# Performance work log

Measured on AMD Instinct MI355X. Metric: run time of the kernel, lower is better.

Reference implementation:

```python
import jax, jax.numpy as jnp
import numpy as np

B, T, D = 16, 4096, 768          # batch, tokens, hidden
N_BOX = 1024                      # total boxes across batch
MAX_BBOX = 128                    # cfg.MODEL.MAX_BBOX_NUM
DIM_DETR = 256                    # DETR feature dim (features[:,1:])


def _lin(k, din, dout):
    kw, kb = jax.random.split(k)
    s = 1.0 / np.sqrt(din)
    W = jax.random.uniform(kw, (dout, din), minval=-s, maxval=s, dtype=jnp.float32)
    b = jax.random.uniform(kb, (dout,), minval=-s, maxval=s, dtype=jnp.float32)
    return W, b


def setup_inputs() -> dict:
    key = jax.random.key(0)
    ks = jax.random.split(key, 10)
    inputs = jax.random.normal(ks[0], (B, T, D), dtype=jnp.float32)
    img = jnp.sort(jax.random.randint(ks[1], (N_BOX,), 0, B))
    rest = jax.random.randint(ks[2], (N_BOX, 4), 0, 224)
    bboxes = jnp.concatenate([img[:, None], rest], axis=1).astype(jnp.int32)
    features = jax.random.normal(ks[3], (N_BOX, 1 + DIM_DETR), dtype=jnp.float32)
    t1w, t1b = _lin(ks[4], D, D)      # transform layer 1
    t2w, t2b = _lin(ks[5], D, D)      # transform layer 2
    d1w, d1b = _lin(ks[6], D, D)      # deep_trans layer 1
    d2w, d2b = _lin(ks[7], D, D)      # deep_trans layer 2
    k8a, k8b = jax.random.split(ks[8])
    m1w, m1b = _lin(k8a, DIM_DETR, D) # mlp layer 1 (256->768)
    m2w, m2b = _lin(k8b, D, D)        # mlp layer 2
    pw, pb = _lin(ks[9], 2 * D, D)    # projection (1536->768)
    return dict(inputs=inputs, bboxes=bboxes, features=features,
                t1w=t1w, t1b=t1b, t2w=t2w, t2b=t2b,
                d1w=d1w, d1b=d1b, d2w=d2w, d2b=d2b,
                m1w=m1w, m1b=m1b, m2w=m2w, m2b=m2b,
                pw=pw, pb=pb)


def reference(inputs, bboxes, features, t1w, t1b, t2w, t2b,
              d1w, d1b, d2w, d2b, m1w, m1b, m2w, m2b, pw, pb):
    x = inputs.mean(axis=1)                                    # [B, D]
    ret_x = jax.nn.relu(x @ d1w.T + d1b) @ d2w.T + d2b         # deep_trans
    xt = jax.nn.relu(x @ t1w.T + t1b) @ t2w.T + t2b            # transform
    img = bboxes[:, 0]                                          # [N] image idx per box
    x_boxes = xt[img]                                           # broadcast image feat to its boxes
    fm = jax.nn.relu(features[:, 1:] @ m1w.T + m1b) @ m2w.T + m2b  # DETR mlp
    h = jnp.concatenate([x_boxes, fm], axis=1) @ pw.T + pb      # [N, D]
    # ragged pad: scatter each box into slot (img, rank-within-image)
    counts = jax.ops.segment_sum(jnp.ones((N_BOX,), jnp.int32), img, num_segments=B)
    offsets = jnp.cumsum(counts) - counts                       # exclusive cumsum (boxes sorted by img)
    pos = jnp.arange(N_BOX) - offsets[img]
    vis_output = jnp.zeros((B, MAX_BBOX, D), h.dtype).at[img, pos].set(h)
    att_mask = (jnp.arange(MAX_BBOX)[None, :] < counts[:, None]).astype(jnp.float32)
    return vis_output, att_mask, ret_x
```

## Files before the change

### kernel.cpp

```cpp
#include <hip/hip_runtime.h>

#define B_ 16
#define T_ 4096
#define D_ 768
#define NBOX 1024
#define MAXBB 128
#define DDETR 256

typedef unsigned short u16;
typedef short bf16x8 __attribute__((ext_vector_type(8)));
typedef float f32x4 __attribute__((ext_vector_type(4)));

__device__ __forceinline__ void split_bf(float f, u16& h, u16& l) {
    unsigned u = __builtin_bit_cast(unsigned, f);
    unsigned r = u + 0x7fffu + ((u >> 16) & 1u);
    u16 hb = (u16)(r >> 16);
    float hf = __builtin_bit_cast(float, (unsigned)hb << 16);
    float lf = f - hf;
    unsigned ul = __builtin_bit_cast(unsigned, lf);
    unsigned rl = ul + 0x7fffu + ((ul >> 16) & 1u);
    h = hb; l = (u16)(rl >> 16);
}

__global__ __launch_bounds__(192) void k_mean_partial(const float4* __restrict__ in4,
                                                      float4* __restrict__ part4) {
    int blk = blockIdx.x;
    int b = blk >> 6, c = blk & 63;
    int t = threadIdx.x;
    const float4* base = in4 + (size_t)b * (T_ * D_ / 4) + (size_t)c * (64 * D_ / 4);
    float4 s = {0.f, 0.f, 0.f, 0.f};
    #pragma unroll 4
    for (int r = 0; r < 64; ++r) {
        float4 v = base[(size_t)r * 192 + t];
        s.x += v.x; s.y += v.y; s.z += v.z; s.w += v.w;
    }
    part4[(size_t)blk * 192 + t] = s;
}

struct WDesc { const float* src; u16* hi; u16* lo; int N; int K; int stride; int vec; };
struct WPack8 { WDesc d[8]; };

__global__ __launch_bounds__(256) void k_pack_all(WPack8 ws, const float* __restrict__ part,
                                                  u16* __restrict__ xph, u16* __restrict__ xpl) {
    __shared__ float xm[768];
    if (blockIdx.y == 8) {
        if (blockIdx.x >= 16) return;
        int b = blockIdx.x;
        int t = threadIdx.x;
        if (t < 192) {
            f32x4 s = {0.f, 0.f, 0.f, 0.f};
            #pragma unroll 4
            for (int c = 0; c < 64; ++c)
                s += *(const f32x4*)(part + ((size_t)(b * 64 + c)) * 768 + t * 4);
            s *= (1.0f / T_);
            *(f32x4*)(xm + t * 4) = s;
        }
        __syncthreads();
        if (t < 96) {
            const float* p = xm + t * 8;
            bf16x8 hv, lv;
            #pragma unroll
            for (int j = 0; j < 8; ++j) {
                u16 h, l;
                split_bf(p[j], h, l); hv[j] = (short)h; lv[j] = (short)l;
            }
            size_t off = ((size_t)t * 16 + b) * 8;
            *(bf16x8*)(xph + off) = hv;
            *(bf16x8*)(xpl + off) = lv;
        }
        return;
    }
    WDesc d = ws.d[blockIdx.y];
    int idx = blockIdx.x * 256 + threadIdx.x;
    int Kc = d.K >> 3;
    int total = d.N * Kc;
    if (idx >= total) return;
    int n = idx / Kc, kc = idx - n * Kc;
    const float* s = d.src + (size_t)n * d.stride + kc * 8;
    float v[8];
    if (d.vec) {
        f32x4 v0 = *(const f32x4*)s, v1 = *(const f32x4*)(s + 4);
        #pragma unroll
        for (int j = 0; j < 4; ++j) { v[j] = v0[j]; v[4 + j] = v1[j]; }
    } else {
        #pragma unroll
        for (int j = 0; j < 8; ++j) v[j] = s[j];
    }
    bf16x8 hv, lv;
    #pragma unroll
    for (int j = 0; j < 8; ++j) {
        u16 h, l;
        split_bf(v[j], h, l); hv[j] = (short)h; lv[j] = (short)l;
    }
    size_t off = ((size_t)(n >> 4) * Kc + kc) * 128 + (n & 15) * 8;
    *(bf16x8*)(d.hi + off) = hv;
    *(bf16x8*)(d.lo + off) = lv;
}

template<int GATHER>
__global__ __launch_bounds__(256) void k_mfma(const u16* __restrict__ Ahi, const u16* __restrict__ Alo,
                                              const u16* __restrict__ Whi, const u16* __restrict__ Wlo,
                                              const u16* __restrict__ Xth, const u16* __restrict__ Xtl,
                                              const int* __restrict__ bbx,
                                              float* __restrict__ P, int Kc, int kcLen, int nks) {
    int z = blockIdx.z;
    int term = z / nks, ks = z - term * nks;
    int lane = threadIdx.x & 63, w = threadIdx.x >> 6;
    int wm = w >> 1, wn = w & 1;
    int mt0 = blockIdx.y * 8 + wm * 4;
    int nt0 = blockIdx.x * 8 + wn * 4;
    int kc0 = ks * kcLen;
    int nk = kcLen >> 2;

    const u16* W = (term == 1) ? Wlo : Whi;
    const u16* Wp = W + ((size_t)nt0 * Kc + kc0) * 128 + lane * 8;
    size_t wstr = (size_t)Kc * 128;

    const u16* Abase;
    size_t aofs[4];
    if (GATHER && ks == 0) {
        Abase = (term == 2) ? Xtl : Xth;
        #pragma unroll
        for (int i = 0; i < 4; ++i) {
            int row = (mt0 + i) * 16 + (lane & 15);
            aofs[i] = (size_t)(lane >> 4) * 128 + (size_t)bbx[row * 5] * 8;
        }
    } else {
        int AKc = GATHER ? 96 : Kc;
        int kc0a = GATHER ? 0 : kc0;
        Abase = (term == 2) ? Alo : Ahi;
        #pragma unroll
        for (int i = 0; i < 4; ++i)
            aofs[i] = ((size_t)(mt0 + i) * AKc + kc0a) * 128 + lane * 8;
    }

    bf16x8 a[4], b[4];
    #pragma unroll
    for (int i = 0; i < 4; ++i) {
        a[i] = *(const bf16x8*)(Abase + aofs[i]);
        b[i] = *(const bf16x8*)(Wp + i * wstr);
    }
    f32x4 acc[16];
    #pragma unroll
    for (int i = 0; i < 16; ++i) acc[i] = (f32x4){0.f, 0.f, 0.f, 0.f};

    for (int k = 0; k < nk; ++k) {
        bf16x8 an[4], bn[4];
        if (k + 1 < nk) {
            #pragma unroll
            for (int i = 0; i < 4; ++i) {
                an[i] = *(const bf16x8*)(Abase + aofs[i] + (size_t)(k + 1) * 512);
                bn[i] = *(const bf16x8*)(Wp + i * wstr + (size_t)(k + 1) * 512);
            }
        }
        #pragma unroll
        for (int i = 0; i < 4; ++i)
            #pragma unroll
            for (int j = 0; j < 4; ++j)
                acc[i * 4 + j] = __builtin_amdgcn_mfma_f32_16x16x32_bf16(a[i], b[j], acc[i * 4 + j], 0, 0, 0);
        #pragma unroll
        for (int i = 0; i < 4; ++i) { a[i] = an[i]; b[i] = bn[i]; }
    }

    float* Pz = P + (size_t)z * (1024 * 768);
    int rb = (lane >> 4) * 4, cb = lane & 15;
    #pragma unroll
    for (int i = 0; i < 4; ++i)
        #pragma unroll
        for (int j = 0; j < 4; ++j) {
            int row = (mt0 + i) * 16 + rb;
            int col = (nt0 + j) * 16 + cb;
            float* p = Pz + (size_t)row * 768 + col;
            f32x4 v = acc[i * 4 + j];
            #pragma unroll
            for (int r = 0; r < 4; ++r) p[(size_t)r * 768] = v[r];
        }
}

template<int RELU>
__global__ __launch_bounds__(256) void k_epi_pack(const float* __restrict__ P, int NS,
                                                  const float* __restrict__ bias,
                                                  u16* __restrict__ dhi, u16* __restrict__ dlo,
                                                  int KcDst, int kcOff) {
    int idx = blockIdx.x * 256 + threadIdx.x;
    int m = idx / 96, kc = idx - m * 96;
    const float* p0 = P + (size_t)m * 768 + kc * 8;
    f32x4 s0 = *(const f32x4*)p0, s1 = *(const f32x4*)(p0 + 4);
    for (int z = 1; z < NS; ++z) {
        const float* p = p0 + (size_t)z * (1024 * 768);
        s0 += *(const f32x4*)p; s1 += *(const f32x4*)(p + 4);
    }
    s0 += *(const f32x4*)(bias + kc * 8);
    s1 += *(const f32x4*)(bias + kc * 8 + 4);
    bf16x8 hv, lv;
    #pragma unroll
    for (int j = 0; j < 4; ++j) {
        float v0 = RELU ? fmaxf(s0[j], 0.f) : s0[j];
        float v1 = RELU ? fmaxf(s1[j], 0.f) : s1[j];
        u16 h, l;
        split_bf(v0, h, l); hv[j] = (short)h; lv[j] = (short)l;
        split_bf(v1, h, l); hv[4 + j] = (short)h; lv[4 + j] = (short)l;
    }
    size_t off = ((size_t)(m >> 4) * KcDst + kcOff + kc) * 128 + (m & 15) * 8;
    *(bf16x8*)(dhi + off) = hv;
    *(bf16x8*)(dlo + off) = lv;
}

__global__ __launch_bounds__(256) void k_epi_vis(const float* __restrict__ P, int NS,
                                                 const float* __restrict__ bias,
                                                 float* __restrict__ vis,
                                                 const int* __restrict__ bbx,
                                                 const int* __restrict__ off) {
    int idx = blockIdx.x * 256 + threadIdx.x;
    int m = idx / 192, c4 = idx - m * 192;
    size_t o = (size_t)m * 768 + c4 * 4;
    f32x4 s = *(const f32x4*)(P + o);
    for (int z = 1; z < NS; ++z) s += *(const f32x4*)(P + (size_t)z * (1024 * 768) + o);
    s += *(const f32x4*)(bias + c4 * 4);
    int b = bbx[m * 5];
    int pp = m - off[b];
    if (pp < MAXBB)
        *(f32x4*)&vis[((size_t)(b * MAXBB + pp)) * 768 + c4 * 4] = s;
}

__global__ __launch_bounds__(256) void k_small(const u16* __restrict__ A0h, const u16* __restrict__ A0l,
                                               const u16* __restrict__ A1h, const u16* __restrict__ A1l,
                                               const u16* __restrict__ W0h, const u16* __restrict__ W0l,
                                               const u16* __restrict__ W1h, const u16* __restrict__ W1l,
                                               float* __restrict__ Ps) {
    int z = blockIdx.y;
    int term = z >> 2, ks = z & 3;
    int lane = threadIdx.x & 63, w = threadIdx.x >> 6;
    int nt0 = blockIdx.x * 16 + w * 4;
    int path = nt0 >= 48;
    int ntp = nt0 - path * 48;
    const u16* Ah = path ? A1h : A0h;
    const u16* Al = path ? A1l : A0l;
    const u16* Wh = path ? W1h : W0h;
    const u16* Wl = path ? W1l : W0l;
    const u16* A = (term == 2) ? Al : Ah;
    const u16* W = (term == 1) ? Wl : Wh;
    int kc0 = ks * 24;

    const u16* Ap = A + (size_t)kc0 * 128 + lane * 8;
    const u16* Wp = W + ((size_t)ntp * 96 + kc0) * 128 + lane * 8;

    f32x4 acc[4];
    #pragma unroll
    for (int i = 0; i < 4; ++i) acc[i] = (f32x4){0.f, 0.f, 0.f, 0.f};

    #pragma unroll
    for (int k = 0; k < 6; ++k) {
        bf16x8 a = *(const bf16x8*)(Ap + (size_t)k * 512);
        bf16x8 b[4];
        #pragma unroll
        for (int j = 0; j < 4; ++j)
            b[j] = *(const bf16x8*)(Wp + (size_t)j * 96 * 128 + (size_t)k * 512);
        #pragma unroll
        for (int j = 0; j < 4; ++j)
            acc[j] = __builtin_amdgcn_mfma_f32_16x16x32_bf16(a, b[j], acc[j], 0, 0, 0);
    }

    float* Pz = Ps + (size_t)z * (16 * 1536);
    int rb = (lane >> 4) * 4, cb = lane & 15;
    #pragma unroll
    for (int j = 0; j < 4; ++j) {
        int col = (nt0 + j) * 16 + cb;
        float* p = Pz + (size_t)rb * 1536 + col;
        f32x4 v = acc[j];
        #pragma unroll
        for (int r = 0; r < 4; ++r) p[(size_t)r * 1536] = v[r];
    }
}

__global__ __launch_bounds__(256) void k_sepi1(const float* __restrict__ Ps,
                                               const float* __restrict__ d1b, const float* __restrict__ t1b,
                                               u16* __restrict__ xh, u16* __restrict__ xl) {
    int idx = blockIdx.x * 256 + threadIdx.x;
    int r = idx / 192, cc = idx - r * 192;
    size_t base = (size_t)r * 1536 + cc * 8;
    f32x4 s0 = {0,0,0,0}, s1 = {0,0,0,0};
    for (int z = 0; z < 12; ++z) {
        const float* p = Ps + (size_t)z * (16 * 1536) + base;
        s0 += *(const f32x4*)p; s1 += *(const f32x4*)(p + 4);
    }
    int path = cc >= 96;
    int ccp = cc - path * 96;
    const float* bias = (path ? t1b : d1b) + ccp * 8;
    s0 += *(const f32x4*)bias;
    s1 += *(const f32x4*)(bias + 4);
    bf16x8 hv, lv;
    #pragma unroll
    for (int j = 0; j < 4; ++j) {
        u16 h, l;
        split_bf(fmaxf(s0[j], 0.f), h, l); hv[j] = (short)h; lv[j] = (short)l;
        split_bf(fmaxf(s1[j], 0.f), h, l); hv[4 + j] = (short)h; lv[4 + j] = (short)l;
    }
    size_t off = (size_t)path * 12288 + (size_t)ccp * 128 + r * 8;
    *(bf16x8*)(xh + off) = hv;
    *(bf16x8*)(xl + off) = lv;
}

__global__ __launch_bounds__(256) void k_sepi2(const float* __restrict__ Ps,
                                               const float* __restrict__ d2b, const float* __restrict__ t2b,
                                               float* __restrict__ retx,
                                               u16* __restrict__ xth, u16* __restrict__ xtl) {
    int idx = blockIdx.x * 256 + threadIdx.x;
    int r = idx / 192, cc = idx - r * 192;
    size_t base = (size_t)r * 1536 + cc * 8;
    f32x4 s0 = {0,0,0,0}, s1 = {0,0,0,0};
    for (int z = 0; z < 12; ++z) {
        const float* p = Ps + (size_t)z * (16 * 1536) + base;
        s0 += *(const f32x4*)p; s1 += *(const f32x4*)(p + 4);
    }
    int path = cc >= 96;
    int ccp = cc - path * 96;
    const float* bias = (path ? t2b : d2b) + ccp * 8;
    s0 += *(const f32x4*)bias;
    s1 += *(const f32x4*)(bias + 4);
    if (!path) {
        float* o = retx + (size_t)r * 768 + ccp * 8;
        *(f32x4*)o = s0;
        *(f32x4*)(o + 4) = s1;
    } else {
        bf16x8 hv, lv;
        #pragma unroll
        for (int j = 0; j < 4; ++j) {
            u16 h, l;
            split_bf(s0[j], h, l); hv[j] = (short)h; lv[j] = (short)l;
            split_bf(s1[j], h, l); hv[4 + j] = (short)h; lv[4 + j] = (short)l;
        }
        size_t off = (size_t)ccp * 128 + r * 8;
        *(bf16x8*)(xth + off) = hv;
        *(bf16x8*)(xtl + off) = lv;
    }
}

__global__ __launch_bounds__(256) void k_meta_vz(const int* __restrict__ bboxes,
                                                 int* __restrict__ cnt_g, int* __restrict__ off_g,
                                                 float* __restrict__ att, f32x4* __restrict__ vis4) {
    if (blockIdx.x > 0) {
        int idx = (blockIdx.x - 1) * 256 + threadIdx.x;
        vis4[idx] = (f32x4){0.f, 0.f, 0.f, 0.f};
        return;
    }
    __shared__ int cnt[B_];
    __shared__ int off[B_];
    int tid = threadIdx.x;
    if (tid < B_) cnt[tid] = 0;
    __syncthreads();
    for (int i = tid; i < NBOX; i += 256) atomicAdd(&cnt[bboxes[i * 5]], 1);
    __syncthreads();
    if (tid == 0) {
        int acc = 0;
        for (int b = 0; b < B_; ++b) { off[b] = acc; acc += cnt[b]; }
    }
    __syncthreads();
    if (tid < B_) { cnt_g[tid] = cnt[tid]; off_g[tid] = off[tid]; }
    for (int j = tid; j < B_ * MAXBB; j += 256) {
        int b = j >> 7, p = j & 127;
        att[j] = (p < cnt[b]) ? 1.0f : 0.0f;
    }
}

extern "C" void kernel_launch(void* const* d_in, const int* in_sizes, int n_in,
                              void* d_out, int out_size, void* d_ws, size_t ws_size,
                              hipStream_t stream) {
    const float* inputs   = (const float*)d_in[0];
    const int*   bboxes   = (const int*)d_in[1];
    const float* features = (const float*)d_in[2];
    const float* t1w = (const float*)d_in[3];
    const float* t1b = (const float*)d_in[4];
    const float* t2w = (const float*)d_in[5];
    const float* t2b = (const float*)d_in[6];
    const float* d1w = (const float*)d_in[7];
    const float* d1b = (const float*)d_in[8];
    const float* d2w = (const float*)d_in[9];
    const float* d2b = (const float*)d_in[10];
    const float* m1w = (const float*)d_in[11];
    const float* m1b = (const float*)d_in[12];
    const float* m2w = (const float*)d_in[13];
    const float* m2b = (const float*)d_in[14];
    const float* pw  = (const float*)d_in[15];
    const float* pb  = (const float*)d_in[16];

    float* out  = (float*)d_out;
    float* vis  = out;
    float* att  = out + 1572864;
    float* retx = out + 1574912;

    float* wsf  = (float*)d_ws;
    float* part = wsf;
    float* P    = wsf + 786432;
    float* Ps   = P + 6 * 786432;
    int*   cnt  = (int*)(Ps + 294912);
    int*   off  = cnt + 16;
    u16*   sb   = (u16*)(off + 48);

    u16* t1wh = sb;              u16* t1wl = t1wh + 589824;
    u16* t2wh = t1wl + 589824;   u16* t2wl = t2wh + 589824;
    u16* d1wh = t2wl + 589824;   u16* d1wl = d1wh + 589824;
    u16* d2wh = d1wl + 589824;   u16* d2wl = d2wh + 589824;
    u16* m1wh = d2wl + 589824;   u16* m1wl = m1wh + 196608;
    u16* m2wh = m1wl + 196608;   u16* m2wl = m2wh + 589824;
    u16* pwh  = m2wl + 589824;   u16* pwl  = pwh + 1179648;
    u16* feah = pwl + 1179648;   u16* feal = feah + 262144;
    u16* fm1h = feal + 262144;   u16* fm1l = fm1h + 786432;
    u16* fmh  = fm1l + 786432;   u16* fml  = fmh + 786432;
    u16* xph  = fml + 786432;    u16* xpl  = xph + 12288;
    u16* xch  = xpl + 12288;     u16* xcl  = xch + 24576;
    u16* xth  = xcl + 24576;     u16* xtl  = xth + 12288;

    k_meta_vz<<<1537, 256, 0, stream>>>(bboxes, cnt, off, att, (f32x4*)vis);

    k_mean_partial<<<B_ * 64, 192, 0, stream>>>((const float4*)inputs, (float4*)part);

    WPack8 wp;
    wp.d[0] = {t1w, t1wh, t1wl, 768, 768, 768, 1};
    wp.d[1] = {t2w, t2wh, t2wl, 768, 768, 768, 1};
    wp.d[2] = {d1w, d1wh, d1wl, 768, 768, 768, 1};
    wp.d[3] = {d2w, d2wh, d2wl, 768, 768, 768, 1};
    wp.d[4] = {m1w, m1wh, m1wl, 768, 256, 256, 1};
    wp.d[5] = {m2w, m2wh, m2wl, 768, 768, 768, 1};
    wp.d[6] = {pw,  pwh,  pwl,  768, 1536, 1536, 1};
    wp.d[7] = {features + 1, feah, feal, 1024, 256, 257, 0};
    k_pack_all<<<dim3(576, 9), 256, 0, stream>>>(wp, part, xph, xpl);

    k_small<<<dim3(6, 12), 256, 0, stream>>>(xph, xpl, xph, xpl,
                                             d1wh, d1wl, t1wh, t1wl, Ps);
    k_sepi1<<<12, 256, 0, stream>>>(Ps, d1b, t1b, xch, xcl);
    k_small<<<dim3(6, 12), 256, 0, stream>>>(xch, xcl, xch + 12288, xcl + 12288,
                                             d2wh, d2wl, t2wh, t2wl, Ps);
    k_sepi2<<<12, 256, 0, stream>>>(Ps, d2b, t2b, retx, xth, xtl);

    k_mfma<0><<<dim3(6, 8, 3), 256, 0, stream>>>(feah, feal, m1wh, m1wl,
                                                 nullptr, nullptr, nullptr, P, 32, 32, 1);
    k_epi_pack<1><<<384, 256, 0, stream>>>(P, 3, m1b, fm1h, fm1l, 96, 0);

    k_mfma<0><<<dim3(6, 8, 6), 256, 0, stream>>>(fm1h, fm1l, m2wh, m2wl,
                                                 nullptr, nullptr, nullptr, P, 96, 48, 2);
    k_epi_pack<0><<<384, 256, 0, stream>>>(P, 6, m2b, fmh, fml, 96, 0);

    k_mfma<1><<<dim3(6, 8, 6), 256, 0, stream>>>(fmh, fml, pwh, pwl,
                                                 xth, xtl, bboxes, P, 192, 96, 2);
    k_epi_vis<<<768, 256, 0, stream>>>(P, 6, pb, vis, bboxes, off);
}
```

Measured before the change: 408.8 us.

## Merge independent kernels into phase kernels and drop split-K for MLP GEMMs

Combines the mean-partial, meta/zero-fill and weight-pack kernels into one front kernel, and pairs the small deep/transform GEMMs with the DETR MLP GEMMs and their epilogues in shared phase launches. This cuts the launch count from about 13 to 8 and lets independent work share the GPU. The MFMA GEMMs no longer use split-K, so each block walks the full K range and the partial buffer shrinks to three terms. The gather GEMM now switches between xt and fm sources inside its K loop. The trade-off is fewer blocks per GEMM and longer serial K loops, which may lower parallelism on the big GEMMs.

```diff
diff --git a/kernel.cpp b/kernel.cpp
--- a/kernel.cpp
+++ b/kernel.cpp
@@ -22,56 +22,58 @@
     h = hb; l = (u16)(rl >> 16);
 }
 
-__global__ __launch_bounds__(192) void k_mean_partial(const float4* __restrict__ in4,
-                                                      float4* __restrict__ part4) {
-    int blk = blockIdx.x;
-    int b = blk >> 6, c = blk & 63;
-    int t = threadIdx.x;
-    const float4* base = in4 + (size_t)b * (T_ * D_ / 4) + (size_t)c * (64 * D_ / 4);
-    float4 s = {0.f, 0.f, 0.f, 0.f};
-    #pragma unroll 4
-    for (int r = 0; r < 64; ++r) {
-        float4 v = base[(size_t)r * 192 + t];
-        s.x += v.x; s.y += v.y; s.z += v.z; s.w += v.w;
-    }
-    part4[(size_t)blk * 192 + t] = s;
-}
-
 struct WDesc { const float* src; u16* hi; u16* lo; int N; int K; int stride; int vec; };
 struct WPack8 { WDesc d[8]; };
 
-__global__ __launch_bounds__(256) void k_pack_all(WPack8 ws, const float* __restrict__ part,
-                                                  u16* __restrict__ xph, u16* __restrict__ xpl) {
-    __shared__ float xm[768];
-    if (blockIdx.y == 8) {
-        if (blockIdx.x >= 16) return;
-        int b = blockIdx.x;
-        int t = threadIdx.x;
-        if (t < 192) {
-            f32x4 s = {0.f, 0.f, 0.f, 0.f};
-            #pragma unroll 4
-            for (int c = 0; c < 64; ++c)
-                s += *(const f32x4*)(part + ((size_t)(b * 64 + c)) * 768 + t * 4);
-            s *= (1.0f / T_);
-            *(f32x4*)(xm + t * 4) = s;
-        }
+__global__ __launch_bounds__(256) void k_front(WPack8 ws,
+                                               const float4* __restrict__ in4,
+                                               float4* __restrict__ part4,
+                                               const int* __restrict__ bboxes,
+                                               int* __restrict__ cnt_g, int* __restrict__ off_g,
+                                               float* __restrict__ att, f32x4* __restrict__ vis4) {
+    int bx = blockIdx.x;
+    int tid = threadIdx.x;
+    if (bx < 1024) {
+        if (tid >= 192) return;
+        int b = bx >> 6, c = bx & 63;
+        const float4* base = in4 + (size_t)b * (T_ * D_ / 4) + (size_t)c * (64 * D_ / 4);
+        float4 s = {0.f, 0.f, 0.f, 0.f};
+        #pragma unroll 4
+        for (int r = 0; r < 64; ++r) {
+            float4 v = base[(size_t)r * 192 + tid];
+            s.x += v.x; s.y += v.y; s.z += v.z; s.w += v.w;
+        }
+        part4[(size_t)bx * 192 + tid] = s;
+        return;
+    }
+    if (bx < 2561) {
+        int mb = bx - 1024;
+        if (mb > 0) {
+            int idx = (mb - 1) * 256 + tid;
+            vis4[idx] = (f32x4){0.f, 0.f, 0.f, 0.f};
+            return;
+        }
+        __shared__ int cnt[B_];
+        __shared__ int off[B_];
+        if (tid < B_) cnt[tid] = 0;
         __syncthreads();
-        if (t < 96) {
-            const float* p = xm + t * 8;
-            bf16x8 hv, lv;
-            #pragma unroll
-            for (int j = 0; j < 8; ++j) {
-                u16 h, l;
-                split_bf(p[j], h, l); hv[j] = (short)h; lv[j] = (short)l;
-            }
-            size_t off = ((size_t)t * 16 + b) * 8;
-            *(bf16x8*)(xph + off) = hv;
-            *(bf16x8*)(xpl + off) = lv;
+        for (int i = tid; i < NBOX; i += 256) atomicAdd(&cnt[bboxes[i * 5]], 1);
+        __syncthreads();
+        if (tid == 0) {
+            int acc = 0;
+            for (int b = 0; b < B_; ++b) { off[b] = acc; acc += cnt[b]; }
+        }
+        __syncthreads();
+        if (tid < B_) { cnt_g[tid] = cnt[tid]; off_g[tid] = off[tid]; }
+        for (int j = tid; j < B_ * MAXBB; j += 256) {
+            int b = j >> 7, p = j & 127;
+            att[j] = (p < cnt[b]) ? 1.0f : 0.0f;
         }
         return;
     }
-    WDesc d = ws.d[blockIdx.y];
-    int idx = blockIdx.x * 256 + threadIdx.x;
+    int pidx = bx - 2561;
+    WDesc d = ws.d[pidx / 576];
+    int idx = (pidx % 576) * 256 + tid;
     int Kc = d.K >> 3;
     int total = d.N * Kc;
     if (idx >= total) return;
@@ -97,49 +99,84 @@
     *(bf16x8*)(d.lo + off) = lv;
 }
 
+__global__ __launch_bounds__(256) void k_mean_final(const float* __restrict__ part,
+                                                    u16* __restrict__ xph, u16* __restrict__ xpl) {
+    __shared__ float xm[768];
+    int b = blockIdx.x;
+    int t = threadIdx.x;
+    if (t < 192) {
+        f32x4 s = {0.f, 0.f, 0.f, 0.f};
+        #pragma unroll 4
+        for (int c = 0; c < 64; ++c)
+            s += *(const f32x4*)(part + ((size_t)(b * 64 + c)) * 768 + t * 4);
+        s *= (1.0f / T_);
+        *(f32x4*)(xm + t * 4) = s;
+    }
+    __syncthreads();
+    if (t < 96) {
+        const float* p = xm + t * 8;
+        bf16x8 hv, lv;
+        #pragma unroll
+        for (int j = 0; j < 8; ++j) {
+            u16 h, l;
+            split_bf(p[j], h, l); hv[j] = (short)h; lv[j] = (short)l;
+        }
+        size_t off = ((size_t)t * 16 + b) * 8;
+        *(bf16x8*)(xph + off) = hv;
+        *(bf16x8*)(xpl + off) = lv;
+    }
+}
+
 template<int GATHER>
-__global__ __launch_bounds__(256) void k_mfma(const u16* __restrict__ Ahi, const u16* __restrict__ Alo,
-                                              const u16* __restrict__ Whi, const u16* __restrict__ Wlo,
-                                              const u16* __restrict__ Xth, const u16* __restrict__ Xtl,
-                                              const int* __restrict__ bbx,
-                                              float* __restrict__ P, int Kc, int kcLen, int nks) {
-    int z = blockIdx.z;
-    int term = z / nks, ks = z - term * nks;
-    int lane = threadIdx.x & 63, w = threadIdx.x >> 6;
+__device__ __forceinline__ void dev_mfma(const u16* __restrict__ Ahi, const u16* __restrict__ Alo,
+                                         const u16* __restrict__ Whi, const u16* __restrict__ Wlo,
+                                         const u16* __restrict__ Xth, const u16* __restrict__ Xtl,
+                                         const int* __restrict__ bbx,
+                                         float* __restrict__ P, int Kc,
+                                         int bxn, int byn, int term, int tid) {
+    int lane = tid & 63, w = tid >> 6;
     int wm = w >> 1, wn = w & 1;
-    int mt0 = blockIdx.y * 8 + wm * 4;
-    int nt0 = blockIdx.x * 8 + wn * 4;
-    int kc0 = ks * kcLen;
-    int nk = kcLen >> 2;
+    int mt0 = byn * 8 + wm * 4;
+    int nt0 = bxn * 8 + wn * 4;
+    int nk = Kc >> 2;
 
     const u16* W = (term == 1) ? Wlo : Whi;
-    const u16* Wp = W + ((size_t)nt0 * Kc + kc0) * 128 + lane * 8;
+    const u16* Wp = W + ((size_t)nt0 * Kc) * 128 + lane * 8;
     size_t wstr = (size_t)Kc * 128;
 
-    const u16* Abase;
-    size_t aofs[4];
-    if (GATHER && ks == 0) {
-        Abase = (term == 2) ? Xtl : Xth;
+    const u16* Ab = (term == 2) ? Alo : Ahi;
+    const u16* Xb = (term == 2) ? Xtl : Xth;
+    int AKc = GATHER ? 96 : Kc;
+    size_t aofs[4], xofs[4];
+    #pragma unroll
+    for (int i = 0; i < 4; ++i)
+        aofs[i] = ((size_t)(mt0 + i) * AKc) * 128 + lane * 8;
+    if (GATHER) {
         #pragma unroll
         for (int i = 0; i < 4; ++i) {
             int row = (mt0 + i) * 16 + (lane & 15);
-            aofs[i] = (size_t)(lane >> 4) * 128 + (size_t)bbx[row * 5] * 8;
-        }
-    } else {
-        int AKc = GATHER ? 96 : Kc;
-        int kc0a = GATHER ? 0 : kc0;
-        Abase = (term == 2) ? Alo : Ahi;
-        #pragma unroll
-        for (int i = 0; i < 4; ++i)
-            aofs[i] = ((size_t)(mt0 + i) * AKc + kc0a) * 128 + lane * 8;
-    }
+            xofs[i] = (size_t)(lane >> 4) * 128 + (size_t)bbx[row * 5] * 8;
+        }
+    }
+
+    auto LA = [&](int k, bf16x8 (&a)[4]) {
+        if (GATHER && k < 24) {
+            #pragma unroll
+            for (int i = 0; i < 4; ++i)
+                a[i] = *(const bf16x8*)(Xb + xofs[i] + (size_t)k * 512);
+        } else {
+            int kk = GATHER ? k - 24 : k;
+            #pragma unroll
+            for (int i = 0; i < 4; ++i)
+                a[i] = *(const bf16x8*)(Ab + aofs[i] + (size_t)kk * 512);
+        }
+    };
 
     bf16x8 a[4], b[4];
-    #pragma unroll
-    for (int i = 0; i < 4; ++i) {
-        a[i] = *(const bf16x8*)(Abase + aofs[i]);
-        b[i] = *(const bf16x8*)(Wp + i * wstr);
-    }
+    LA(0, a);
+    #pragma unroll
+    for (int i = 0; i < 4; ++i) b[i] = *(const bf16x8*)(Wp + i * wstr);
+
     f32x4 acc[16];
     #pragma unroll
     for (int i = 0; i < 16; ++i) acc[i] = (f32x4){0.f, 0.f, 0.f, 0.f};
@@ -147,11 +184,10 @@
     for (int k = 0; k < nk; ++k) {
         bf16x8 an[4], bn[4];
         if (k + 1 < nk) {
+            LA(k + 1, an);
             #pragma unroll
-            for (int i = 0; i < 4; ++i) {
-                an[i] = *(const bf16x8*)(Abase + aofs[i] + (size_t)(k + 1) * 512);
+            for (int i = 0; i < 4; ++i)
                 bn[i] = *(const bf16x8*)(Wp + i * wstr + (size_t)(k + 1) * 512);
-            }
         }
         #pragma unroll
         for (int i = 0; i < 4; ++i)
@@ -162,7 +198,7 @@
         for (int i = 0; i < 4; ++i) { a[i] = an[i]; b[i] = bn[i]; }
     }
 
-    float* Pz = P + (size_t)z * (1024 * 768);
+    float* Pz = P + (size_t)term * (1024 * 768);
     int rb = (lane >> 4) * 4, cb = lane & 15;
     #pragma unroll
     for (int i = 0; i < 4; ++i)
@@ -177,16 +213,17 @@
         }
 }
 
-template<int RELU>
-__global__ __launch_bounds__(256) void k_epi_pack(const float* __restrict__ P, int NS,
-                                                  const float* __restrict__ bias,
-                                                  u16* __restrict__ dhi, u16* __restrict__ dlo,
-                                                  int KcDst, int kcOff) {
-    int idx = blockIdx.x * 256 + threadIdx.x;
+__device__ __forceinline__ void dev_epi_pack(int blk, int tid, int relu,
+                                             const float* __restrict__ P,
+                                             const float* __restrict__ bias,
+                                             u16* __restrict__ dhi, u16* __restrict__ dlo,
+                                             int KcDst, int kcOff) {
+    int idx = blk * 256 + tid;
     int m = idx / 96, kc = idx - m * 96;
     const float* p0 = P + (size_t)m * 768 + kc * 8;
     f32x4 s0 = *(const f32x4*)p0, s1 = *(const f32x4*)(p0 + 4);
-    for (int z = 1; z < NS; ++z) {
+    #pragma unroll
+    for (int z = 1; z < 3; ++z) {
         const float* p = p0 + (size_t)z * (1024 * 768);
         s0 += *(const f32x4*)p; s1 += *(const f32x4*)(p + 4);
     }
@@ -195,8 +232,8 @@
     bf16x8 hv, lv;
     #pragma unroll
     for (int j = 0; j < 4; ++j) {
-        float v0 = RELU ? fmaxf(s0[j], 0.f) : s0[j];
-        float v1 = RELU ? fmaxf(s1[j], 0.f) : s1[j];
+        float v0 = relu ? fmaxf(s0[j], 0.f) : s0[j];
+        float v1 = relu ? fmaxf(s1[j], 0.f) : s1[j];
         u16 h, l;
         split_bf(v0, h, l); hv[j] = (short)h; lv[j] = (short)l;
         split_bf(v1, h, l); hv[4 + j] = (short)h; lv[4 + j] = (short)l;
@@ -206,7 +243,7 @@
     *(bf16x8*)(dlo + off) = lv;
 }
 
-__global__ __launch_bounds__(256) void k_epi_vis(const float* __restrict__ P, int NS,
+__global__ __launch_bounds__(256) void k_epi_vis(const float* __restrict__ P,
                                                  const float* __restrict__ bias,
                                                  float* __restrict__ vis,
                                                  const int* __restrict__ bbx,
@@ -215,7 +252,8 @@
     int m = idx / 192, c4 = idx - m * 192;
     size_t o = (size_t)m * 768 + c4 * 4;
     f32x4 s = *(const f32x4*)(P + o);
-    for (int z = 1; z < NS; ++z) s += *(const f32x4*)(P + (size_t)z * (1024 * 768) + o);
+    #pragma unroll
+    for (int z = 1; z < 3; ++z) s += *(const f32x4*)(P + (size_t)z * (1024 * 768) + o);
     s += *(const f32x4*)(bias + c4 * 4);
     int b = bbx[m * 5];
     int pp = m - off[b];
@@ -223,15 +261,15 @@
         *(f32x4*)&vis[((size_t)(b * MAXBB + pp)) * 768 + c4 * 4] = s;
 }
 
-__global__ __launch_bounds__(256) void k_small(const u16* __restrict__ A0h, const u16* __restrict__ A0l,
-                                               const u16* __restrict__ A1h, const u16* __restrict__ A1l,
-                                               const u16* __restrict__ W0h, const u16* __restrict__ W0l,
-                                               const u16* __restrict__ W1h, const u16* __restrict__ W1l,
-                                               float* __restrict__ Ps) {
-    int z = blockIdx.y;
+__device__ __forceinline__ void dev_small(int bxn, int z, int tid,
+                                          const u16* __restrict__ A0h, const u16* __restrict__ A0l,
+                                          const u16* __restrict__ A1h, const u16* __restrict__ A1l,
+                                          const u16* __restrict__ W0h, const u16* __restrict__ W0l,
+                                          const u16* __restrict__ W1h, const u16* __restrict__ W1l,
+                                          float* __restrict__ Ps) {
     int term = z >> 2, ks = z & 3;
-    int lane = threadIdx.x & 63, w = threadIdx.x >> 6;
-    int nt0 = blockIdx.x * 16 + w * 4;
+    int lane = tid & 63, w = tid >> 6;
+    int nt0 = bxn * 16 + w * 4;
     int path = nt0 >= 48;
     int ntp = nt0 - path * 48;
     const u16* Ah = path ? A1h : A0h;
@@ -273,10 +311,11 @@
     }
 }
 
-__global__ __launch_bounds__(256) void k_sepi1(const float* __restrict__ Ps,
-                                               const float* __restrict__ d1b, const float* __restrict__ t1b,
-                                               u16* __restrict__ xh, u16* __restrict__ xl) {
-    int idx = blockIdx.x * 256 + threadIdx.x;
+__device__ __forceinline__ void dev_sepi1(int blk, int tid,
+                                          const float* __restrict__ Ps,
+                                          const float* __restrict__ d1b, const float* __restrict__ t1b,
+                                          u16* __restrict__ xh, u16* __restrict__ xl) {
+    int idx = blk * 256 + tid;
     int r = idx / 192, cc = idx - r * 192;
     size_t base = (size_t)r * 1536 + cc * 8;
     f32x4 s0 = {0,0,0,0}, s1 = {0,0,0,0};
@@ -301,11 +340,12 @@
     *(bf16x8*)(xl + off) = lv;
 }
 
-__global__ __launch_bounds__(256) void k_sepi2(const float* __restrict__ Ps,
-                                               const float* __restrict__ d2b, const float* __restrict__ t2b,
-                                               float* __restrict__ retx,
-                                               u16* __restrict__ xth, u16* __restrict__ xtl) {
-    int idx = blockIdx.x * 256 + threadIdx.x;
+__device__ __forceinline__ void dev_sepi2(int blk, int tid,
+                                          const float* __restrict__ Ps,
+                                          const float* __restrict__ d2b, const float* __restrict__ t2b,
+                                          float* __restrict__ retx,
+                                          u16* __restrict__ xth, u16* __restrict__ xtl) {
+    int idx = blk * 256 + tid;
     int r = idx / 192, cc = idx - r * 192;
     size_t base = (size_t)r * 1536 + cc * 8;
     f32x4 s0 = {0,0,0,0}, s1 = {0,0,0,0};
@@ -336,31 +376,69 @@
     }
 }
 
-__global__ __launch_bounds__(256) void k_meta_vz(const int* __restrict__ bboxes,
-                                                 int* __restrict__ cnt_g, int* __restrict__ off_g,
-                                                 float* __restrict__ att, f32x4* __restrict__ vis4) {
-    if (blockIdx.x > 0) {
-        int idx = (blockIdx.x - 1) * 256 + threadIdx.x;
-        vis4[idx] = (f32x4){0.f, 0.f, 0.f, 0.f};
-        return;
-    }
-    __shared__ int cnt[B_];
-    __shared__ int off[B_];
-    int tid = threadIdx.x;
-    if (tid < B_) cnt[tid] = 0;
-    __syncthreads();
-    for (int i = tid; i < NBOX; i += 256) atomicAdd(&cnt[bboxes[i * 5]], 1);
-    __syncthreads();
-    if (tid == 0) {
-        int acc = 0;
-        for (int b = 0; b < B_; ++b) { off[b] = acc; acc += cnt[b]; }
-    }
-    __syncthreads();
-    if (tid < B_) { cnt_g[tid] = cnt[tid]; off_g[tid] = off[tid]; }
-    for (int j = tid; j < B_ * MAXBB; j += 256) {
-        int b = j >> 7, p = j & 127;
-        att[j] = (p < cnt[b]) ? 1.0f : 0.0f;
-    }
+__global__ __launch_bounds__(256) void k_phaseA(const u16* xph, const u16* xpl,
+                                                const u16* d1wh, const u16* d1wl,
+                                                const u16* t1wh, const u16* t1wl,
+                                                float* Ps,
+                                                const u16* feah, const u16* feal,
+                                                const u16* m1wh, const u16* m1wl,
+                                                float* P) {
+    int bx = blockIdx.x, tid = threadIdx.x;
+    if (bx < 72) {
+        dev_small(bx % 6, bx / 6, tid, xph, xpl, xph, xpl,
+                  d1wh, d1wl, t1wh, t1wl, Ps);
+    } else {
+        int i = bx - 72;
+        dev_mfma<0>(feah, feal, m1wh, m1wl, nullptr, nullptr, nullptr,
+                    P, 32, i % 6, (i / 6) % 8, i / 48, tid);
+    }
+}
+
+__global__ __launch_bounds__(256) void k_phaseB(const float* Ps,
+                                                const float* d1b, const float* t1b,
+                                                u16* xch, u16* xcl,
+                                                const float* P, const float* m1b,
+                                                u16* fm1h, u16* fm1l) {
+    int bx = blockIdx.x, tid = threadIdx.x;
+    if (bx < 12) dev_sepi1(bx, tid, Ps, d1b, t1b, xch, xcl);
+    else dev_epi_pack(bx - 12, tid, 1, P, m1b, fm1h, fm1l, 96, 0);
+}
+
+__global__ __launch_bounds__(256) void k_phaseC(const u16* xch, const u16* xcl,
+                                                const u16* d2wh, const u16* d2wl,
+                                                const u16* t2wh, const u16* t2wl,
+                                                float* Ps,
+                                                const u16* fm1h, const u16* fm1l,
+                                                const u16* m2wh, const u16* m2wl,
+                                                float* P) {
+    int bx = blockIdx.x, tid = threadIdx.x;
+    if (bx < 72) {
+        dev_small(bx % 6, bx / 6, tid, xch, xcl, xch + 12288, xcl + 12288,
+                  d2wh, d2wl, t2wh, t2wl, Ps);
+    } else {
+        int i = bx - 72;
+        dev_mfma<0>(fm1h, fm1l, m2wh, m2wl, nullptr, nullptr, nullptr,
+                    P, 96, i % 6, (i / 6) % 8, i / 48, tid);
+    }
+}
+
+__global__ __launch_bounds__(256) void k_phaseD(const float* Ps,
+                                                const float* d2b, const float* t2b,
+                                                float* retx, u16* xth, u16* xtl,
+                                                const float* P, const float* m2b,
+                                                u16* fmh, u16* fml) {
+    int bx = blockIdx.x, tid = threadIdx.x;
+    if (bx < 12) dev_sepi2(bx, tid, Ps, d2b, t2b, retx, xth, xtl);
+    else dev_epi_pack(bx - 12, tid, 0, P, m2b, fmh, fml, 96, 0);
+}
+
+__global__ __launch_bounds__(256) void k_pw(const u16* fmh, const u16* fml,
+                                            const u16* pwh, const u16* pwl,
+                                            const u16* xth, const u16* xtl,
+                                            const int* bbx, float* P) {
+    int i = blockIdx.x, tid = threadIdx.x;
+    dev_mfma<1>(fmh, fml, pwh, pwl, xth, xtl, bbx,
+                P, 192, i % 6, (i / 6) % 8, i / 48, tid);
 }
 
 extern "C" void kernel_launch(void* const* d_in, const int* in_sizes, int n_in,
@@ -392,7 +470,7 @@
     float* wsf  = (float*)d_ws;
     float* part = wsf;
     float* P    = wsf + 786432;
-    float* Ps   = P + 6 * 786432;
+    float* Ps   = P + 3 * 786432;
     int*   cnt  = (int*)(Ps + 294912);
     int*   off  = cnt + 16;
     u16*   sb   = (u16*)(off + 48);
@@ -411,10 +489,6 @@
     u16* xch  = xpl + 12288;     u16* xcl  = xch + 24576;
     u16* xth  = xcl + 24576;     u16* xtl  = xth + 12288;
 
-    k_meta_vz<<<1537, 256, 0, stream>>>(bboxes, cnt, off, att, (f32x4*)vis);
-
-    k_mean_partial<<<B_ * 64, 192, 0, stream>>>((const float4*)inputs, (float4*)part);
-
     WPack8 wp;
     wp.d[0] = {t1w, t1wh, t1wl, 768, 768, 768, 1};
     wp.d[1] = {t2w, t2wh, t2wl, 768, 768, 768, 1};
@@ -424,24 +498,22 @@
     wp.d[5] = {m2w, m2wh, m2wl, 768, 768, 768, 1};
     wp.d[6] = {pw,  pwh,  pwl,  768, 1536, 1536, 1};
     wp.d[7] = {features + 1, feah, feal, 1024, 256, 257, 0};
-    k_pack_all<<<dim3(576, 9), 256, 0, stream>>>(wp, part, xph, xpl);
-
-    k_small<<<dim3(6, 12), 256, 0, stream>>>(xph, xpl, xph, xpl,
-                                             d1wh, d1wl, t1wh, t1wl, Ps);
-    k_sepi1<<<12, 256, 0, stream>>>(Ps, d1b, t1b, xch, xcl);
-    k_small<<<dim3(6, 12), 256, 0, stream>>>(xch, xcl, xch + 12288, xcl + 12288,
-                                             d2wh, d2wl, t2wh, t2wl, Ps);
-    k_sepi2<<<12, 256, 0, stream>>>(Ps, d2b, t2b, retx, xth, xtl);
-
-    k_mfma<0><<<dim3(6, 8, 3), 256, 0, stream>>>(feah, feal, m1wh, m1wl,
-                                                 nullptr, nullptr, nullptr, P, 32, 32, 1);
-    k_epi_pack<1><<<384, 256, 0, stream>>>(P, 3, m1b, fm1h, fm1l, 96, 0);
-
-    k_mfma<0><<<dim3(6, 8, 6), 256, 0, stream>>>(fm1h, fm1l, m2wh, m2wl,
-                                                 nullptr, nullptr, nullptr, P, 96, 48, 2);
-    k_epi_pack<0><<<384, 256, 0, stream>>>(P, 6, m2b, fmh, fml, 96, 0);
-
-    k_mfma<1><<<dim3(6, 8, 6), 256, 0, stream>>>(fmh, fml, pwh, pwl,
-                                                 xth, xtl, bboxes, P, 192, 96, 2);
-    k_epi_vis<<<768, 256, 0, stream>>>(P, 6, pb, vis, bboxes, off);
-}
+    k_front<<<7169, 256, 0, stream>>>(wp, (const float4*)inputs, (float4*)part,
+                                      bboxes, cnt, off, att, (f32x4*)vis);
+
+    k_mean_final<<<16, 256, 0, stream>>>(part, xph, xpl);
+
+    k_phaseA<<<216, 256, 0, stream>>>(xph, xpl, d1wh, d1wl, t1wh, t1wl, Ps,
+                                      feah, feal, m1wh, m1wl, P);
+
+    k_phaseB<<<396, 256, 0, stream>>>(Ps, d1b, t1b, xch, xcl, P, m1b, fm1h, fm1l);
+
+    k_phaseC<<<216, 256, 0, stream>>>(xch, xcl, d2wh, d2wl, t2wh, t2wl, Ps,
+                                      fm1h, fm1l, m2wh, m2wl, P);
+
+    k_phaseD<<<396, 256, 0, stream>>>(Ps, d2b, t2b, retx, xth, xtl, P, m2b, fmh, fml);
+
+    k_pw<<<144, 256, 0, stream>>>(fmh, fml, pwh, pwl, xth, xtl, bboxes, P);
+
+    k_epi_vis<<<768, 256, 0, stream>>>(P, pb, vis, bboxes, off);
+}
```

New measurement: 404.7 us. About the same (-1.0%).
